# Kernel optimization log

Hardware: AMD Instinct MI355X
Metric: run time of the kernel (lower is better)

Reference implementation:

```python
import jax, jax.numpy as jnp
import numpy as np

DELTA = 0.1625
FREQ_SCALE = 0.325
MIN_LAYERS = 1
MAX_LAYERS = 5
EPS = 1e-12  # F.normalize eps


def _l2norm(x, axis):
    n = jnp.sqrt(jnp.sum(x * x, axis=axis, keepdims=True))
    return x / jnp.maximum(n, EPS)


def setup_inputs() -> dict:
    key = jax.random.key(0)
    k1, k2, k3 = jax.random.split(key, 3)
    B, N, D = 8, 2048, 64
    embeddings = jax.random.normal(k1, (B, N, D), dtype=jnp.float32)
    # scale to [0, 15) so echo_layers spans the full 1..5 range
    frequencies = jax.random.uniform(k2, (B, N), dtype=jnp.float32) * 15.0
    relationship_matrix = jax.random.uniform(k3, (B, N, N), dtype=jnp.float32)
    return {"embeddings": embeddings, "frequencies": frequencies,
            "relationship_matrix": relationship_matrix}


def reference(embeddings, frequencies, relationship_matrix):
    B, N, D = embeddings.shape
    # per-token number of echo iterations
    echo_layers = jnp.clip(
        MIN_LAYERS + jnp.floor(frequencies * FREQ_SCALE), MIN_LAYERS, MAX_LAYERS
    ).astype(jnp.int32)  # [B, N]

    refined = _l2norm(embeddings, axis=2)  # [B, N, D]

    # mask out the diagonal of the relationship matrix once (it is constant
    # across layers); shifts[i] = delta * sum_j rm[i,j]*(e_i - e_j)
    #               = delta * (e_i * rowsum[i] - (rm @ e)[i])
    rm = relationship_matrix * (1.0 - jnp.eye(N, dtype=relationship_matrix.dtype))
    rowsum = jnp.sum(rm, axis=-1)  # [B, N]

    def step(e, layer):
        active = (layer < echo_layers)[..., None].astype(e.dtype)  # [B, N, 1]
        agg = jnp.einsum('bij,bjd->bid', rm, e)                     # [B, N, D]
        shifts = DELTA * (e * rowsum[..., None] - agg)
        upd = _l2norm(e + shifts * active, axis=2)
        # tokens with zero shift are already unit-norm, so renorm is identity
        return upd, None

    refined, _ = jax.lax.scan(step, refined, jnp.arange(MAX_LAYERS))
    return refined
```

## Files before the change

kernel.cpp:

```cpp
#include <hip/hip_runtime.h>
#include <stdint.h>

#define BB 8
#define NN 2048
#define DD 64
#define DELTA 0.1625f
#define FREQ_SCALE 0.325f

typedef __bf16 bf16x8 __attribute__((ext_vector_type(8)));
typedef float f32x4 __attribute__((ext_vector_type(4)));
typedef unsigned int u32x4 __attribute__((ext_vector_type(4)));
typedef unsigned int u32x2 __attribute__((ext_vector_type(2)));

static __device__ __forceinline__ unsigned short f2b(float x) {
    union { float f; unsigned int u; } c; c.f = x;
    unsigned int r = (c.u + 0x7FFFu + ((c.u >> 16) & 1u)) >> 16;
    return (unsigned short)r;
}

static __device__ __forceinline__ void gl_lds16(const void* g, void* l) {
    __builtin_amdgcn_global_load_lds(
        (const __attribute__((address_space(1))) void*)g,
        (__attribute__((address_space(3))) void*)l, 16, 0, 0);
}

__global__ __launch_bounds__(256) void prep_norm(
        const float* __restrict__ emb, const float* __restrict__ freq,
        float* __restrict__ e0, unsigned short* __restrict__ eT0,
        int* __restrict__ echo) {
    __shared__ unsigned short tile[64][72];
    int t = threadIdx.x;
    int tok0 = blockIdx.x * 64;
    int lt = t >> 2;
    int tt = tok0 + lt;
    int dd = (t & 3) * 16;

    const float* src = emb + (size_t)tt * DD + dd;
    f32x4 v[4];
    float ss = 0.f;
    #pragma unroll
    for (int q = 0; q < 4; q++) {
        v[q] = *(const f32x4*)(src + q * 4);
        ss += v[q].x*v[q].x + v[q].y*v[q].y + v[q].z*v[q].z + v[q].w*v[q].w;
    }
    ss += __shfl_xor(ss, 1);
    ss += __shfl_xor(ss, 2);
    float scale = 1.f / fmaxf(sqrtf(ss), 1e-12f);
    float* dst = e0 + (size_t)tt * DD + dd;
    #pragma unroll
    for (int q = 0; q < 4; q++) {
        f32x4 o = v[q] * scale;
        *(f32x4*)(dst + q * 4) = o;
        tile[lt][dd + q*4 + 0] = f2b(o.x);
        tile[lt][dd + q*4 + 1] = f2b(o.y);
        tile[lt][dd + q*4 + 2] = f2b(o.z);
        tile[lt][dd + q*4 + 3] = f2b(o.w);
    }
    if ((t & 3) == 0) {
        int el = 1 + (int)floorf(freq[tt] * FREQ_SCALE);
        el = el < 1 ? 1 : (el > 5 ? 5 : el);
        echo[tt] = el;
    }
    __syncthreads();
    int b  = tok0 / NN;
    int tb = tok0 % NN;
    for (int idx = t; idx < 64 * 64; idx += 256) {
        int d = idx >> 6, j = idx & 63;
        eT0[((size_t)b * DD + d) * NN + tb + j] = tile[j][d];
    }
}

template<bool WRB>
__global__ __launch_bounds__(256) void cast_rowsum(
        const float* __restrict__ rm, unsigned short* __restrict__ rmb,
        float* __restrict__ rowsum) {
    int gw = (int)((blockIdx.x * 256 + threadIdx.x) >> 6);
    int l = threadIdx.x & 63;
    const float* src = rm + (size_t)gw * NN;
    f32x4 v[8];
    #pragma unroll
    for (int q = 0; q < 8; q++)
        v[q] = *(const f32x4*)(src + q * 256 + l * 4);
    float s = 0.f;
    #pragma unroll
    for (int q = 0; q < 8; q++)
        s += (v[q].x + v[q].y) + (v[q].z + v[q].w);
    if constexpr (WRB) {
        unsigned short* dst = rmb + (size_t)gw * NN;
        #pragma unroll
        for (int q = 0; q < 8; q++) {
            u32x2 o;
            o.x = (unsigned)f2b(v[q].x) | ((unsigned)f2b(v[q].y) << 16);
            o.y = (unsigned)f2b(v[q].z) | ((unsigned)f2b(v[q].w) << 16);
            *(u32x2*)(dst + q * 256 + l * 4) = o;
        }
    }
    #pragma unroll
    for (int m = 1; m < 64; m <<= 1) s += __shfl_xor(s, m);
    if (l == 0) rowsum[gw] = s;
}

__global__ __launch_bounds__(512, 1) void layer0_fused(
        const float* __restrict__ rm,
        const unsigned short* __restrict__ eT_src,
        const float* __restrict__ e_src,
        const int* __restrict__ echo,
        unsigned short* __restrict__ rmb_out,
        float* __restrict__ rowsum_out,
        float* __restrict__ e_dst,
        unsigned short* __restrict__ eT_dst) {
    __shared__ char F4[4][16384];
    __shared__ char C4[4][8192];
    __shared__ char SA4[4][8192];
    __shared__ float redSS[4][2][16];
    __shared__ float rsumL[64];

    const int t = threadIdx.x;
    const int w = t >> 6, l = t & 63;
    const int lo = l & 15, hi = l >> 4;
    const int it = w & 3, dh = w >> 2;
    const int gid = blockIdx.x;
    const int b  = gid & 7;
    const int i0 = (gid >> 3) * 64;

    const char* rmB = (const char*)(rm + ((size_t)b * NN + i0) * NN);
    const char* eTB = (const char*)(eT_src + (size_t)b * DD * NN);

    const size_t frow0 = (size_t)(w * 8 + (l >> 4)) * (NN * 4);
    const size_t frow4 = (size_t)(w * 8 + 4 + (l >> 4)) * (NN * 4);
    const int fcs0 = (((l & 15) ^ (l >> 4)) << 4);
    const int fcs4 = (((l & 15) ^ (4 + (l >> 4))) << 4);
    const size_t srowE = (size_t)(w * 8 + (l >> 3)) * (NN * 2);
    const int csrcE = (((l & 7) ^ (l >> 3)) << 4);

    const int rl = w * 8 + (l >> 3);
    const int cs0 = ((2 * (l & 7)) ^ (l >> 3)) << 4;
    const int cs1 = ((2 * (l & 7) + 1) ^ (l >> 3)) << 4;
    const int cdst = rl * 128 + ((((l & 7) ^ (l >> 3))) << 4);
    unsigned short* rmbW = rmb_out + ((size_t)b * NN + i0 + rl) * NN + (l & 7) * 8;

    f32x4 acc0 = {}, acc1 = {};
    float rsum = 0.f;

    const int rowB  = it * 16 + lo;
    const int rowA0 = dh * 32 + lo;
    const int rowA1 = dh * 32 + 16 + lo;
    const int xr = (lo & 7) << 4;

#define ISSUE(bi, step) do {                                        \
    const int kf = (step) * 256;                                    \
    const int ke = (step) * 128;                                    \
    gl_lds16(rmB + frow0 + kf + fcs0, &F4[bi][w * 2048]);           \
    gl_lds16(rmB + frow4 + kf + fcs4, &F4[bi][w * 2048 + 1024]);    \
    gl_lds16(eTB + srowE + ke + csrcE, &SA4[bi][w * 1024]);         \
} while (0)

#define CONVERT(bi, step) do {                                      \
    f32x4 va = *(const f32x4*)(&F4[bi][rl * 256 + cs0]);            \
    f32x4 vb = *(const f32x4*)(&F4[bi][rl * 256 + cs1]);            \
    u32x4 o;                                                        \
    o.x = (unsigned)f2b(va.x) | ((unsigned)f2b(va.y) << 16);        \
    o.y = (unsigned)f2b(va.z) | ((unsigned)f2b(va.w) << 16);        \
    o.z = (unsigned)f2b(vb.x) | ((unsigned)f2b(vb.y) << 16);        \
    o.w = (unsigned)f2b(vb.z) | ((unsigned)f2b(vb.w) << 16);        \
    *(u32x4*)(&C4[bi][cdst]) = o;                                   \
    *(u32x4*)(rmbW + (step) * 64) = o;                              \
    rsum += (va.x + va.y + va.z + va.w) + (vb.x + vb.y + vb.z + vb.w); \
} while (0)

#define COMP(bi) do {                                               \
    __builtin_amdgcn_s_setprio(1);                                  \
    _Pragma("unroll")                                               \
    for (int kk = 0; kk < 2; kk++) {                                \
        int co = ((kk << 6) | (hi << 4)) ^ xr;                      \
        u32x4 fB  = *(const u32x4*)(&C4[bi][rowB  * 128 + co]);     \
        u32x4 fA0 = *(const u32x4*)(&SA4[bi][rowA0 * 128 + co]);    \
        u32x4 fA1 = *(const u32x4*)(&SA4[bi][rowA1 * 128 + co]);    \
        acc0 = __builtin_amdgcn_mfma_f32_16x16x32_bf16(             \
            __builtin_bit_cast(bf16x8, fA0), __builtin_bit_cast(bf16x8, fB), acc0, 0, 0, 0); \
        acc1 = __builtin_amdgcn_mfma_f32_16x16x32_bf16(             \
            __builtin_bit_cast(bf16x8, fA1), __builtin_bit_cast(bf16x8, fB), acc1, 0, 0, 0); \
    }                                                               \
    __builtin_amdgcn_s_setprio(0);                                  \
} while (0)

    ISSUE(0, 0);
    ISSUE(1, 1);
    ISSUE(2, 2);
    #pragma unroll
    for (int s = 0; s < 32; s++) {
        if (s == 0)       asm volatile("s_waitcnt vmcnt(6)" ::: "memory");
        else if (s == 1)  asm volatile("s_waitcnt vmcnt(7)" ::: "memory");
        else if (s == 2)  asm volatile("s_waitcnt vmcnt(8)" ::: "memory");
        else if (s < 30)  asm volatile("s_waitcnt vmcnt(9)" ::: "memory");
        else if (s == 30) asm volatile("s_waitcnt vmcnt(6)" ::: "memory");
        else              asm volatile("s_waitcnt vmcnt(3)" ::: "memory");
        __builtin_amdgcn_s_barrier();
        __builtin_amdgcn_sched_barrier(0);
        if (s < 29) {
            const int nb = (s + 3) & 3;
            if (nb == 0)      ISSUE(0, s + 3);
            else if (nb == 1) ISSUE(1, s + 3);
            else if (nb == 2) ISSUE(2, s + 3);
            else              ISSUE(3, s + 3);
        }
        const int cb = s & 3;
        if (cb == 0)      CONVERT(0, s);
        else if (cb == 1) CONVERT(1, s);
        else if (cb == 2) CONVERT(2, s);
        else              CONVERT(3, s);
        asm volatile("s_waitcnt lgkmcnt(0)" ::: "memory");
        __builtin_amdgcn_sched_barrier(0);
        __builtin_amdgcn_s_barrier();
        if (cb == 0)      COMP(0);
        else if (cb == 1) COMP(1);
        else if (cb == 2) COMP(2);
        else              COMP(3);
    }
#undef ISSUE
#undef CONVERT
#undef COMP

    rsum += __shfl_xor(rsum, 1);
    rsum += __shfl_xor(rsum, 2);
    rsum += __shfl_xor(rsum, 4);
    if ((l & 7) == 0) {
        rsumL[rl] = rsum;
        rowsum_out[(size_t)b * NN + i0 + rl] = rsum;
    }
    __syncthreads();

    const size_t gi = (size_t)b * NN + i0 + it * 16 + lo;
    const float rs = rsumL[it * 16 + lo];
    const float coef = (0 < echo[gi]) ? DELTA : 0.f;
    const size_t eb = gi * DD + dh * 32 + hi * 4;
    f32x4 e0 = *(const f32x4*)(e_src + eb);
    f32x4 e1 = *(const f32x4*)(e_src + eb + 16);
    f32x4 u0 = e0 + coef * (e0 * rs - acc0);
    f32x4 u1 = e1 + coef * (e1 * rs - acc1);
    float ss = u0.x*u0.x + u0.y*u0.y + u0.z*u0.z + u0.w*u0.w
             + u1.x*u1.x + u1.y*u1.y + u1.z*u1.z + u1.w*u1.w;
    ss += __shfl_xor(ss, 16);
    ss += __shfl_xor(ss, 32);
    if (hi == 0) redSS[it][dh][lo] = ss;
    __syncthreads();
    float sst = redSS[it][0][lo] + redSS[it][1][lo];
    float scale = 1.f / fmaxf(sqrtf(sst), 1e-12f);
    u0 *= scale;
    u1 *= scale;
    *(f32x4*)(e_dst + eb) = u0;
    *(f32x4*)(e_dst + eb + 16) = u1;
    unsigned short* ep = eT_dst + (size_t)b * DD * NN;
    const int i = i0 + it * 16 + lo;
    const int d0 = dh * 32 + hi * 4;
    ep[(size_t)(d0 + 0)  * NN + i] = f2b(u0.x);
    ep[(size_t)(d0 + 1)  * NN + i] = f2b(u0.y);
    ep[(size_t)(d0 + 2)  * NN + i] = f2b(u0.z);
    ep[(size_t)(d0 + 3)  * NN + i] = f2b(u0.w);
    ep[(size_t)(d0 + 16) * NN + i] = f2b(u1.x);
    ep[(size_t)(d0 + 17) * NN + i] = f2b(u1.y);
    ep[(size_t)(d0 + 18) * NN + i] = f2b(u1.z);
    ep[(size_t)(d0 + 19) * NN + i] = f2b(u1.w);
}

__global__ __launch_bounds__(512, 1) void layer_fused(
        const unsigned short* __restrict__ rmb,
        const unsigned short* __restrict__ eT_src,
        const float* __restrict__ e_src,
        const float* __restrict__ rowsum_g,
        const int* __restrict__ echo,
        float* __restrict__ e_dst,
        unsigned short* __restrict__ eT_dst,
        int layer) {
    __shared__ char SB6[6][8192];
    __shared__ char SA6[6][8192];
    __shared__ float redSS[4][2][16];

    const int t = threadIdx.x;
    const int w = t >> 6, l = t & 63;
    const int lo = l & 15, hi = l >> 4;
    const int it = w & 3, dh = w >> 2;
    const int gid = blockIdx.x;
    const int b  = gid & 7;
    const int i0 = (gid >> 3) * 64;

    const char* rmB = (const char*)(rmb + ((size_t)b * NN + i0) * NN);
    const char* eTB = (const char*)(eT_src + (size_t)b * DD * NN);

    const size_t srow = (size_t)(w * 8 + (l >> 3)) * (NN * 2);
    const int csrc = ((l & 7) ^ (l >> 3)) << 4;

    f32x4 acc0 = {}, acc1 = {};

    const int rowB  = it * 16 + lo;
    const int rowA0 = dh * 32 + lo;
    const int rowA1 = dh * 32 + 16 + lo;
    const int xr = (lo & 7) << 4;

#define ISSUE(bi, step) do {                                       \
    const int ksb = (step) * 128;                                  \
    gl_lds16(rmB + srow + ksb + csrc, &SB6[bi][w * 1024]);         \
    gl_lds16(eTB + srow + ksb + csrc, &SA6[bi][w * 1024]);         \
} while (0)

#define COMP(bi) do {                                              \
    __builtin_amdgcn_s_setprio(1);                                 \
    _Pragma("unroll")                                              \
    for (int kk = 0; kk < 2; kk++) {                               \
        int co = ((kk << 6) | (hi << 4)) ^ xr;                     \
        u32x4 fB  = *(const u32x4*)(&SB6[bi][rowB  * 128 + co]);   \
        u32x4 fA0 = *(const u32x4*)(&SA6[bi][rowA0 * 128 + co]);   \
        u32x4 fA1 = *(const u32x4*)(&SA6[bi][rowA1 * 128 + co]);   \
        acc0 = __builtin_amdgcn_mfma_f32_16x16x32_bf16(            \
            __builtin_bit_cast(bf16x8, fA0), __builtin_bit_cast(bf16x8, fB), acc0, 0, 0, 0); \
        acc1 = __builtin_amdgcn_mfma_f32_16x16x32_bf16(            \
            __builtin_bit_cast(bf16x8, fA1), __builtin_bit_cast(bf16x8, fB), acc1, 0, 0, 0); \
    }                                                              \
    __builtin_amdgcn_s_setprio(0);                                 \
} while (0)

    ISSUE(0, 0);
    ISSUE(1, 1);
    ISSUE(2, 2);
    ISSUE(3, 3);
    ISSUE(4, 4);
    #pragma unroll
    for (int s = 0; s < 32; s++) {
        if (s < 29)       asm volatile("s_waitcnt vmcnt(8)" ::: "memory");
        else if (s == 29) asm volatile("s_waitcnt vmcnt(4)" ::: "memory");
        else if (s == 30) asm volatile("s_waitcnt vmcnt(2)" ::: "memory");
        else              asm volatile("s_waitcnt vmcnt(0)" ::: "memory");
        __builtin_amdgcn_s_barrier();
        __builtin_amdgcn_sched_barrier(0);
        if (s < 27) {
            const int nb = (s + 5) % 6;
            if (nb == 0)      ISSUE(0, s + 5);
            else if (nb == 1) ISSUE(1, s + 5);
            else if (nb == 2) ISSUE(2, s + 5);
            else if (nb == 3) ISSUE(3, s + 5);
            else if (nb == 4) ISSUE(4, s + 5);
            else              ISSUE(5, s + 5);
        }
        const int cb = s % 6;
        if (cb == 0)      COMP(0);
        else if (cb == 1) COMP(1);
        else if (cb == 2) COMP(2);
        else if (cb == 3) COMP(3);
        else if (cb == 4) COMP(4);
        else              COMP(5);
    }
#undef ISSUE
#undef COMP

    const size_t gi = (size_t)b * NN + i0 + it * 16 + lo;
    const float rs = rowsum_g[gi];
    const float coef = (layer < echo[gi]) ? DELTA : 0.f;
    const size_t eb = gi * DD + dh * 32 + hi * 4;
    f32x4 e0 = *(const f32x4*)(e_src + eb);
    f32x4 e1 = *(const f32x4*)(e_src + eb + 16);
    f32x4 u0 = e0 + coef * (e0 * rs - acc0);
    f32x4 u1 = e1 + coef * (e1 * rs - acc1);
    float ss = u0.x*u0.x + u0.y*u0.y + u0.z*u0.z + u0.w*u0.w
             + u1.x*u1.x + u1.y*u1.y + u1.z*u1.z + u1.w*u1.w;
    ss += __shfl_xor(ss, 16);
    ss += __shfl_xor(ss, 32);
    if (hi == 0) redSS[it][dh][lo] = ss;
    __syncthreads();
    float sst = redSS[it][0][lo] + redSS[it][1][lo];
    float scale = 1.f / fmaxf(sqrtf(sst), 1e-12f);
    u0 *= scale;
    u1 *= scale;
    *(f32x4*)(e_dst + eb) = u0;
    *(f32x4*)(e_dst + eb + 16) = u1;
    unsigned short* ep = eT_dst + (size_t)b * DD * NN;
    const int i = i0 + it * 16 + lo;
    const int d0 = dh * 32 + hi * 4;
    ep[(size_t)(d0 + 0)  * NN + i] = f2b(u0.x);
    ep[(size_t)(d0 + 1)  * NN + i] = f2b(u0.y);
    ep[(size_t)(d0 + 2)  * NN + i] = f2b(u0.z);
    ep[(size_t)(d0 + 3)  * NN + i] = f2b(u0.w);
    ep[(size_t)(d0 + 16) * NN + i] = f2b(u1.x);
    ep[(size_t)(d0 + 17) * NN + i] = f2b(u1.y);
    ep[(size_t)(d0 + 18) * NN + i] = f2b(u1.z);
    ep[(size_t)(d0 + 19) * NN + i] = f2b(u1.w);
}

__global__ __launch_bounds__(512, 4) void layer_step_fb(
        const float* __restrict__ rm_,
        const unsigned short* __restrict__ eT_src,
        const float* __restrict__ e_src,
        const float* __restrict__ rowsum_g,
        const int* __restrict__ echo,
        float* __restrict__ e_dst,
        unsigned short* __restrict__ eT_dst,
        int layer) {
    __shared__ float redAcc[3][2][64][20];

    int t = threadIdx.x;
    int w = t >> 6, l = t & 63;
    int b = blockIdx.y;
    int i0 = blockIdx.x * 32;
    int wi = w & 1;
    int kq = w >> 1;
    int lane_lo = l & 15, lane_hi = l >> 4;
    int i = i0 + wi * 16 + lane_lo;
    size_t gi = (size_t)b * NN + i;
    int kbase = kq * (NN / 4) + 8 * lane_hi;

    int echo_pre = echo[gi];
    float rs = rowsum_g[gi];

    const unsigned short* eT_b = eT_src + (size_t)b * DD * NN;
    const unsigned short* ea0 = eT_b + (size_t)(lane_lo)      * NN + kbase;
    const unsigned short* ea1 = eT_b + (size_t)(16 + lane_lo) * NN + kbase;
    const unsigned short* ea2 = eT_b + (size_t)(32 + lane_lo) * NN + kbase;
    const unsigned short* ea3 = eT_b + (size_t)(48 + lane_lo) * NN + kbase;

    f32x4 acc[4] = {};
    const float* rmp32 = rm_ + gi * NN + kbase;

    #pragma unroll
    for (int j = 0; j < 16; j++) {
        const int o = 32 * j;
        f32x4 lo4 = *(const f32x4*)(rmp32 + o);
        f32x4 hi4 = *(const f32x4*)(rmp32 + o + 4);
        u32x4 ob;
        ob.x = (unsigned)f2b(lo4.x) | ((unsigned)f2b(lo4.y) << 16);
        ob.y = (unsigned)f2b(lo4.z) | ((unsigned)f2b(lo4.w) << 16);
        ob.z = (unsigned)f2b(hi4.x) | ((unsigned)f2b(hi4.y) << 16);
        ob.w = (unsigned)f2b(hi4.z) | ((unsigned)f2b(hi4.w) << 16);
        bf16x8 bfrag = __builtin_bit_cast(bf16x8, ob);
        acc[0] = __builtin_amdgcn_mfma_f32_16x16x32_bf16(
            __builtin_bit_cast(bf16x8, *(const u32x4*)(ea0 + o)), bfrag, acc[0], 0, 0, 0);
        acc[1] = __builtin_amdgcn_mfma_f32_16x16x32_bf16(
            __builtin_bit_cast(bf16x8, *(const u32x4*)(ea1 + o)), bfrag, acc[1], 0, 0, 0);
        acc[2] = __builtin_amdgcn_mfma_f32_16x16x32_bf16(
            __builtin_bit_cast(bf16x8, *(const u32x4*)(ea2 + o)), bfrag, acc[2], 0, 0, 0);
        acc[3] = __builtin_amdgcn_mfma_f32_16x16x32_bf16(
            __builtin_bit_cast(bf16x8, *(const u32x4*)(ea3 + o)), bfrag, acc[3], 0, 0, 0);
    }

    if (kq > 0) {
        #pragma unroll
        for (int f = 0; f < 4; f++)
            *(f32x4*)(&redAcc[kq - 1][wi][l][4 * f]) = acc[f];
    }
    __syncthreads();
    if (kq == 0) {
        #pragma unroll
        for (int f = 0; f < 4; f++) {
            acc[f] += *(const f32x4*)(&redAcc[0][wi][l][4 * f]);
            acc[f] += *(const f32x4*)(&redAcc[1][wi][l][4 * f]);
            acc[f] += *(const f32x4*)(&redAcc[2][wi][l][4 * f]);
        }
        float coef = DELTA * ((layer < echo_pre) ? 1.f : 0.f);
        size_t ebase = gi * DD;
        f32x4 upd[4];
        float ss = 0.f;
        #pragma unroll
        for (int f = 0; f < 4; f++) {
            f32x4 e = *(const f32x4*)(e_src + ebase + 16 * f + 4 * lane_hi);
            f32x4 u = e + coef * (e * rs - acc[f]);
            upd[f] = u;
            ss += u.x*u.x + u.y*u.y + u.z*u.z + u.w*u.w;
        }
        ss += __shfl_xor(ss, 16);
        ss += __shfl_xor(ss, 32);
        float scale = 1.f / fmaxf(sqrtf(ss), 1e-12f);
        unsigned short* ep = eT_dst + (size_t)b * DD * NN;
        #pragma unroll
        for (int f = 0; f < 4; f++) {
            f32x4 o = upd[f] * scale;
            *(f32x4*)(e_dst + ebase + 16 * f + 4 * lane_hi) = o;
            int dbase = 16 * f + 4 * lane_hi;
            ep[(size_t)(dbase + 0) * NN + i] = f2b(o.x);
            ep[(size_t)(dbase + 1) * NN + i] = f2b(o.y);
            ep[(size_t)(dbase + 2) * NN + i] = f2b(o.z);
            ep[(size_t)(dbase + 3) * NN + i] = f2b(o.w);
        }
    }
}

extern "C" void kernel_launch(void* const* d_in, const int* in_sizes, int n_in,
                              void* d_out, int out_size, void* d_ws, size_t ws_size,
                              hipStream_t stream) {
    const float* emb  = (const float*)d_in[0];
    const float* freq = (const float*)d_in[1];
    const float* rm   = (const float*)d_in[2];
    float* out = (float*)d_out;
    char* ws = (char*)d_ws;

    const size_t eBytes   = (size_t)BB * NN * DD * 4;
    const size_t eTBytes  = (size_t)BB * DD * NN * 2;
    const size_t bnBytes  = (size_t)BB * NN * 4;
    const size_t rmbBytes = (size_t)BB * NN * NN * 2;
    float* e_f32[2] = { (float*)ws, (float*)(ws + eBytes) };
    unsigned short* eT[2] = { (unsigned short*)(ws + 2*eBytes),
                              (unsigned short*)(ws + 2*eBytes + eTBytes) };
    float* rowsum = (float*)(ws + 2*eBytes + 2*eTBytes);
    int* echo = (int*)(ws + 2*eBytes + 2*eTBytes + bnBytes);
    unsigned short* rmb = (unsigned short*)(ws + 2*eBytes + 2*eTBytes + 2*bnBytes);
    size_t need_cached = 2*eBytes + 2*eTBytes + 2*bnBytes + rmbBytes;

    int cached = (ws_size >= need_cached) ? 1 : 0;

    prep_norm<<<dim3(BB*NN/64), dim3(256), 0, stream>>>(emb, freq, e_f32[0], eT[0], echo);

    if (cached) {
        layer0_fused<<<dim3(256), dim3(512), 0, stream>>>(
            rm, eT[0], e_f32[0], echo, rmb, rowsum, e_f32[1], eT[1]);
        for (int l = 1; l < 5; l++) {
            float* dst = (l == 4) ? out : e_f32[(l + 1) & 1];
            layer_fused<<<dim3(256), dim3(512), 0, stream>>>(
                rmb, eT[l & 1], e_f32[l & 1], rowsum, echo,
                dst, eT[(l + 1) & 1], l);
        }
    } else {
        cast_rowsum<false><<<dim3(BB*NN/4), dim3(256), 0, stream>>>(rm, nullptr, rowsum);
        for (int l = 0; l < 5; l++) {
            float* dst = (l == 4) ? out : e_f32[(l + 1) & 1];
            layer_step_fb<<<dim3(NN/32, BB), dim3(512), 0, stream>>>(
                rm, eT[l & 1], e_f32[l & 1], rowsum, echo,
                dst, eT[(l + 1) & 1], l);
        }
    }
}
```

Measured before the change: 106.7 us.

## Use 2x2 register-blocked MFMA tiles with split-K warps and LDS reduction

Each warp previously computed a 16-row by 32-dim slice over the full K chunk. Now it computes a 32x32 output tile with four accumulators over half of the K chunk, so each LDS fragment feeds two MFMAs. The two K halves are then summed through LDS before the normalize epilogue. Layer 0 also drops the echo lookup, because every token has at least one active layer. The trade-off is an extra barrier, a reduction round trip through LDS, and an epilogue where only half the warps do work.

After: 108.4 us. Within noise of the previous version (+1.5%).

```diff
diff --git a/kernel.cpp b/kernel.cpp
--- a/kernel.cpp
+++ b/kernel.cpp
@@ -11,6 +11,9 @@
 typedef float f32x4 __attribute__((ext_vector_type(4)));
 typedef unsigned int u32x4 __attribute__((ext_vector_type(4)));
 typedef unsigned int u32x2 __attribute__((ext_vector_type(2)));
+
+#define MFMA16(A, B, C) __builtin_amdgcn_mfma_f32_16x16x32_bf16( \
+    __builtin_bit_cast(bf16x8, A), __builtin_bit_cast(bf16x8, B), C, 0, 0, 0)
 
 static __device__ __forceinline__ unsigned short f2b(float x) {
     union { float f; unsigned int u; } c; c.f = x;
@@ -104,7 +107,6 @@
         const float* __restrict__ rm,
         const unsigned short* __restrict__ eT_src,
         const float* __restrict__ e_src,
-        const int* __restrict__ echo,
         unsigned short* __restrict__ rmb_out,
         float* __restrict__ rowsum_out,
         float* __restrict__ e_dst,
@@ -112,13 +114,13 @@
     __shared__ char F4[4][16384];
     __shared__ char C4[4][8192];
     __shared__ char SA4[4][8192];
-    __shared__ float redSS[4][2][16];
+    __shared__ float redSS2[2][2][2][16];
     __shared__ float rsumL[64];
 
     const int t = threadIdx.x;
     const int w = t >> 6, l = t & 63;
     const int lo = l & 15, hi = l >> 4;
-    const int it = w & 3, dh = w >> 2;
+    const int ri = w & 1, rd = (w >> 1) & 1, ks = w >> 2;
     const int gid = blockIdx.x;
     const int b  = gid & 7;
     const int i0 = (gid >> 3) * 64;
@@ -139,12 +141,11 @@
     const int cdst = rl * 128 + ((((l & 7) ^ (l >> 3))) << 4);
     unsigned short* rmbW = rmb_out + ((size_t)b * NN + i0 + rl) * NN + (l & 7) * 8;
 
-    f32x4 acc0 = {}, acc1 = {};
+    f32x4 acc00 = {}, acc01 = {}, acc10 = {}, acc11 = {};
     float rsum = 0.f;
 
-    const int rowB  = it * 16 + lo;
-    const int rowA0 = dh * 32 + lo;
-    const int rowA1 = dh * 32 + 16 + lo;
+    const int rowB0 = ri * 32 + lo, rowB1 = ri * 32 + 16 + lo;
+    const int rowA0 = rd * 32 + lo, rowA1 = rd * 32 + 16 + lo;
     const int xr = (lo & 7) << 4;
 
 #define ISSUE(bi, step) do {                                        \
@@ -170,17 +171,15 @@
 
 #define COMP(bi) do {                                               \
     __builtin_amdgcn_s_setprio(1);                                  \
-    _Pragma("unroll")                                               \
-    for (int kk = 0; kk < 2; kk++) {                                \
-        int co = ((kk << 6) | (hi << 4)) ^ xr;                      \
-        u32x4 fB  = *(const u32x4*)(&C4[bi][rowB  * 128 + co]);     \
-        u32x4 fA0 = *(const u32x4*)(&SA4[bi][rowA0 * 128 + co]);    \
-        u32x4 fA1 = *(const u32x4*)(&SA4[bi][rowA1 * 128 + co]);    \
-        acc0 = __builtin_amdgcn_mfma_f32_16x16x32_bf16(             \
-            __builtin_bit_cast(bf16x8, fA0), __builtin_bit_cast(bf16x8, fB), acc0, 0, 0, 0); \
-        acc1 = __builtin_amdgcn_mfma_f32_16x16x32_bf16(             \
-            __builtin_bit_cast(bf16x8, fA1), __builtin_bit_cast(bf16x8, fB), acc1, 0, 0, 0); \
-    }                                                               \
+    const int co = ((ks << 6) | (hi << 4)) ^ xr;                    \
+    u32x4 fB0 = *(const u32x4*)(&C4[bi][rowB0 * 128 + co]);         \
+    u32x4 fB1 = *(const u32x4*)(&C4[bi][rowB1 * 128 + co]);         \
+    u32x4 fA0 = *(const u32x4*)(&SA4[bi][rowA0 * 128 + co]);        \
+    u32x4 fA1 = *(const u32x4*)(&SA4[bi][rowA1 * 128 + co]);        \
+    acc00 = MFMA16(fA0, fB0, acc00);                                \
+    acc01 = MFMA16(fA0, fB1, acc01);                                \
+    acc10 = MFMA16(fA1, fB0, acc10);                                \
+    acc11 = MFMA16(fA1, fB1, acc11);                                \
     __builtin_amdgcn_s_setprio(0);                                  \
 } while (0)
 
@@ -228,39 +227,83 @@
         rsumL[rl] = rsum;
         rowsum_out[(size_t)b * NN + i0 + rl] = rsum;
     }
-    __syncthreads();
-
-    const size_t gi = (size_t)b * NN + i0 + it * 16 + lo;
-    const float rs = rsumL[it * 16 + lo];
-    const float coef = (0 < echo[gi]) ? DELTA : 0.f;
-    const size_t eb = gi * DD + dh * 32 + hi * 4;
-    f32x4 e0 = *(const f32x4*)(e_src + eb);
-    f32x4 e1 = *(const f32x4*)(e_src + eb + 16);
-    f32x4 u0 = e0 + coef * (e0 * rs - acc0);
-    f32x4 u1 = e1 + coef * (e1 * rs - acc1);
-    float ss = u0.x*u0.x + u0.y*u0.y + u0.z*u0.z + u0.w*u0.w
-             + u1.x*u1.x + u1.y*u1.y + u1.z*u1.z + u1.w*u1.w;
-    ss += __shfl_xor(ss, 16);
-    ss += __shfl_xor(ss, 32);
-    if (hi == 0) redSS[it][dh][lo] = ss;
-    __syncthreads();
-    float sst = redSS[it][0][lo] + redSS[it][1][lo];
-    float scale = 1.f / fmaxf(sqrtf(sst), 1e-12f);
-    u0 *= scale;
-    u1 *= scale;
-    *(f32x4*)(e_dst + eb) = u0;
-    *(f32x4*)(e_dst + eb + 16) = u1;
-    unsigned short* ep = eT_dst + (size_t)b * DD * NN;
-    const int i = i0 + it * 16 + lo;
-    const int d0 = dh * 32 + hi * 4;
-    ep[(size_t)(d0 + 0)  * NN + i] = f2b(u0.x);
-    ep[(size_t)(d0 + 1)  * NN + i] = f2b(u0.y);
-    ep[(size_t)(d0 + 2)  * NN + i] = f2b(u0.z);
-    ep[(size_t)(d0 + 3)  * NN + i] = f2b(u0.w);
-    ep[(size_t)(d0 + 16) * NN + i] = f2b(u1.x);
-    ep[(size_t)(d0 + 17) * NN + i] = f2b(u1.y);
-    ep[(size_t)(d0 + 18) * NN + i] = f2b(u1.z);
-    ep[(size_t)(d0 + 19) * NN + i] = f2b(u1.w);
+
+    float* redK = (float*)&F4[0][0];
+    __syncthreads();
+    if (ks == 1) {
+        float* dp = redK + ((ri * 2 + rd) * 64 + l) * 17;
+        #pragma unroll
+        for (int j = 0; j < 4; j++) {
+            dp[j] = acc00[j]; dp[4 + j] = acc01[j];
+            dp[8 + j] = acc10[j]; dp[12 + j] = acc11[j];
+        }
+    }
+    __syncthreads();
+    f32x4 u00, u01, u10, u11;
+    size_t eb0 = 0, eb1 = 0;
+    if (ks == 0) {
+        const float* sp = redK + ((ri * 2 + rd) * 64 + l) * 17;
+        #pragma unroll
+        for (int j = 0; j < 4; j++) {
+            acc00[j] += sp[j]; acc01[j] += sp[4 + j];
+            acc10[j] += sp[8 + j]; acc11[j] += sp[12 + j];
+        }
+        const size_t gi0 = (size_t)b * NN + i0 + ri * 32 + lo;
+        const size_t gi1 = gi0 + 16;
+        const float rs0 = rsumL[ri * 32 + lo];
+        const float rs1 = rsumL[ri * 32 + 16 + lo];
+        eb0 = gi0 * DD + rd * 32 + hi * 4;
+        eb1 = gi1 * DD + rd * 32 + hi * 4;
+        f32x4 e00 = *(const f32x4*)(e_src + eb0);
+        f32x4 e10 = *(const f32x4*)(e_src + eb0 + 16);
+        f32x4 e01 = *(const f32x4*)(e_src + eb1);
+        f32x4 e11 = *(const f32x4*)(e_src + eb1 + 16);
+        u00 = e00 + DELTA * (e00 * rs0 - acc00);
+        u10 = e10 + DELTA * (e10 * rs0 - acc10);
+        u01 = e01 + DELTA * (e01 * rs1 - acc01);
+        u11 = e11 + DELTA * (e11 * rs1 - acc11);
+        float ss0 = u00.x*u00.x + u00.y*u00.y + u00.z*u00.z + u00.w*u00.w
+                  + u10.x*u10.x + u10.y*u10.y + u10.z*u10.z + u10.w*u10.w;
+        float ss1 = u01.x*u01.x + u01.y*u01.y + u01.z*u01.z + u01.w*u01.w
+                  + u11.x*u11.x + u11.y*u11.y + u11.z*u11.z + u11.w*u11.w;
+        ss0 += __shfl_xor(ss0, 16); ss0 += __shfl_xor(ss0, 32);
+        ss1 += __shfl_xor(ss1, 16); ss1 += __shfl_xor(ss1, 32);
+        if (hi == 0) {
+            redSS2[ri][rd][0][lo] = ss0;
+            redSS2[ri][rd][1][lo] = ss1;
+        }
+    }
+    __syncthreads();
+    if (ks == 0) {
+        const float sc0 = 1.f / fmaxf(sqrtf(redSS2[ri][0][0][lo] + redSS2[ri][1][0][lo]), 1e-12f);
+        const float sc1 = 1.f / fmaxf(sqrtf(redSS2[ri][0][1][lo] + redSS2[ri][1][1][lo]), 1e-12f);
+        u00 *= sc0; u10 *= sc0; u01 *= sc1; u11 *= sc1;
+        *(f32x4*)(e_dst + eb0) = u00;
+        *(f32x4*)(e_dst + eb0 + 16) = u10;
+        *(f32x4*)(e_dst + eb1) = u01;
+        *(f32x4*)(e_dst + eb1 + 16) = u11;
+        unsigned short* ep = eT_dst + (size_t)b * DD * NN;
+        const int iA = i0 + ri * 32 + lo;
+        const int iB = iA + 16;
+        const int dA = rd * 32 + hi * 4;
+        const int dB = dA + 16;
+        ep[(size_t)(dA + 0) * NN + iA] = f2b(u00.x);
+        ep[(size_t)(dA + 1) * NN + iA] = f2b(u00.y);
+        ep[(size_t)(dA + 2) * NN + iA] = f2b(u00.z);
+        ep[(size_t)(dA + 3) * NN + iA] = f2b(u00.w);
+        ep[(size_t)(dB + 0) * NN + iA] = f2b(u10.x);
+        ep[(size_t)(dB + 1) * NN + iA] = f2b(u10.y);
+        ep[(size_t)(dB + 2) * NN + iA] = f2b(u10.z);
+        ep[(size_t)(dB + 3) * NN + iA] = f2b(u10.w);
+        ep[(size_t)(dA + 0) * NN + iB] = f2b(u01.x);
+        ep[(size_t)(dA + 1) * NN + iB] = f2b(u01.y);
+        ep[(size_t)(dA + 2) * NN + iB] = f2b(u01.z);
+        ep[(size_t)(dA + 3) * NN + iB] = f2b(u01.w);
+        ep[(size_t)(dB + 0) * NN + iB] = f2b(u11.x);
+        ep[(size_t)(dB + 1) * NN + iB] = f2b(u11.y);
+        ep[(size_t)(dB + 2) * NN + iB] = f2b(u11.z);
+        ep[(size_t)(dB + 3) * NN + iB] = f2b(u11.w);
+    }
 }
 
 __global__ __launch_bounds__(512, 1) void layer_fused(
@@ -274,12 +317,12 @@
         int layer) {
     __shared__ char SB6[6][8192];
     __shared__ char SA6[6][8192];
-    __shared__ float redSS[4][2][16];
+    __shared__ float redSS2[2][2][2][16];
 
     const int t = threadIdx.x;
     const int w = t >> 6, l = t & 63;
     const int lo = l & 15, hi = l >> 4;
-    const int it = w & 3, dh = w >> 2;
+    const int ri = w & 1, rd = (w >> 1) & 1, ks = w >> 2;
     const int gid = blockIdx.x;
     const int b  = gid & 7;
     const int i0 = (gid >> 3) * 64;
@@ -290,11 +333,10 @@
     const size_t srow = (size_t)(w * 8 + (l >> 3)) * (NN * 2);
     const int csrc = ((l & 7) ^ (l >> 3)) << 4;
 
-    f32x4 acc0 = {}, acc1 = {};
-
-    const int rowB  = it * 16 + lo;
-    const int rowA0 = dh * 32 + lo;
-    const int rowA1 = dh * 32 + 16 + lo;
+    f32x4 acc00 = {}, acc01 = {}, acc10 = {}, acc11 = {};
+
+    const int rowB0 = ri * 32 + lo, rowB1 = ri * 32 + 16 + lo;
+    const int rowA0 = rd * 32 + lo, rowA1 = rd * 32 + 16 + lo;
     const int xr = (lo & 7) << 4;
 
 #define ISSUE(bi, step) do {                                       \
@@ -305,17 +347,15 @@
 
 #define COMP(bi) do {                                              \
     __builtin_amdgcn_s_setprio(1);                                 \
-    _Pragma("unroll")                                              \
-    for (int kk = 0; kk < 2; kk++) {                               \
-        int co = ((kk << 6) | (hi << 4)) ^ xr;                     \
-        u32x4 fB  = *(const u32x4*)(&SB6[bi][rowB  * 128 + co]);   \
-        u32x4 fA0 = *(const u32x4*)(&SA6[bi][rowA0 * 128 + co]);   \
-        u32x4 fA1 = *(const u32x4*)(&SA6[bi][rowA1 * 128 + co]);   \
-        acc0 = __builtin_amdgcn_mfma_f32_16x16x32_bf16(            \
-            __builtin_bit_cast(bf16x8, fA0), __builtin_bit_cast(bf16x8, fB), acc0, 0, 0, 0); \
-        acc1 = __builtin_amdgcn_mfma_f32_16x16x32_bf16(            \
-            __builtin_bit_cast(bf16x8, fA1), __builtin_bit_cast(bf16x8, fB), acc1, 0, 0, 0); \
-    }                                                              \
+    const int co = ((ks << 6) | (hi << 4)) ^ xr;                   \
+    u32x4 fB0 = *(const u32x4*)(&SB6[bi][rowB0 * 128 + co]);       \
+    u32x4 fB1 = *(const u32x4*)(&SB6[bi][rowB1 * 128 + co]);       \
+    u32x4 fA0 = *(const u32x4*)(&SA6[bi][rowA0 * 128 + co]);       \
+    u32x4 fA1 = *(const u32x4*)(&SA6[bi][rowA1 * 128 + co]);       \
+    acc00 = MFMA16(fA0, fB0, acc00);                               \
+    acc01 = MFMA16(fA0, fB1, acc01);                               \
+    acc10 = MFMA16(fA1, fB0, acc10);                               \
+    acc11 = MFMA16(fA1, fB1, acc11);                               \
     __builtin_amdgcn_s_setprio(0);                                 \
 } while (0)
 
@@ -352,37 +392,84 @@
 #undef ISSUE
 #undef COMP
 
-    const size_t gi = (size_t)b * NN + i0 + it * 16 + lo;
-    const float rs = rowsum_g[gi];
-    const float coef = (layer < echo[gi]) ? DELTA : 0.f;
-    const size_t eb = gi * DD + dh * 32 + hi * 4;
-    f32x4 e0 = *(const f32x4*)(e_src + eb);
-    f32x4 e1 = *(const f32x4*)(e_src + eb + 16);
-    f32x4 u0 = e0 + coef * (e0 * rs - acc0);
-    f32x4 u1 = e1 + coef * (e1 * rs - acc1);
-    float ss = u0.x*u0.x + u0.y*u0.y + u0.z*u0.z + u0.w*u0.w
-             + u1.x*u1.x + u1.y*u1.y + u1.z*u1.z + u1.w*u1.w;
-    ss += __shfl_xor(ss, 16);
-    ss += __shfl_xor(ss, 32);
-    if (hi == 0) redSS[it][dh][lo] = ss;
-    __syncthreads();
-    float sst = redSS[it][0][lo] + redSS[it][1][lo];
-    float scale = 1.f / fmaxf(sqrtf(sst), 1e-12f);
-    u0 *= scale;
-    u1 *= scale;
-    *(f32x4*)(e_dst + eb) = u0;
-    *(f32x4*)(e_dst + eb + 16) = u1;
-    unsigned short* ep = eT_dst + (size_t)b * DD * NN;
-    const int i = i0 + it * 16 + lo;
-    const int d0 = dh * 32 + hi * 4;
-    ep[(size_t)(d0 + 0)  * NN + i] = f2b(u0.x);
-    ep[(size_t)(d0 + 1)  * NN + i] = f2b(u0.y);
-    ep[(size_t)(d0 + 2)  * NN + i] = f2b(u0.z);
-    ep[(size_t)(d0 + 3)  * NN + i] = f2b(u0.w);
-    ep[(size_t)(d0 + 16) * NN + i] = f2b(u1.x);
-    ep[(size_t)(d0 + 17) * NN + i] = f2b(u1.y);
-    ep[(size_t)(d0 + 18) * NN + i] = f2b(u1.z);
-    ep[(size_t)(d0 + 19) * NN + i] = f2b(u1.w);
+    float* redK = (float*)&SB6[0][0];
+    __syncthreads();
+    if (ks == 1) {
+        float* dp = redK + ((ri * 2 + rd) * 64 + l) * 17;
+        #pragma unroll
+        for (int j = 0; j < 4; j++) {
+            dp[j] = acc00[j]; dp[4 + j] = acc01[j];
+            dp[8 + j] = acc10[j]; dp[12 + j] = acc11[j];
+        }
+    }
+    __syncthreads();
+    f32x4 u00, u01, u10, u11;
+    size_t eb0 = 0, eb1 = 0;
+    if (ks == 0) {
+        const float* sp = redK + ((ri * 2 + rd) * 64 + l) * 17;
+        #pragma unroll
+        for (int j = 0; j < 4; j++) {
+            acc00[j] += sp[j]; acc01[j] += sp[4 + j];
+            acc10[j] += sp[8 + j]; acc11[j] += sp[12 + j];
+        }
+        const size_t gi0 = (size_t)b * NN + i0 + ri * 32 + lo;
+        const size_t gi1 = gi0 + 16;
+        const float rs0 = rowsum_g[gi0];
+        const float rs1 = rowsum_g[gi1];
+        const float c0 = (layer < echo[gi0]) ? DELTA : 0.f;
+        const float c1 = (layer < echo[gi1]) ? DELTA : 0.f;
+        eb0 = gi0 * DD + rd * 32 + hi * 4;
+        eb1 = gi1 * DD + rd * 32 + hi * 4;
+        f32x4 e00 = *(const f32x4*)(e_src + eb0);
+        f32x4 e10 = *(const f32x4*)(e_src + eb0 + 16);
+        f32x4 e01 = *(const f32x4*)(e_src + eb1);
+        f32x4 e11 = *(const f32x4*)(e_src + eb1 + 16);
+        u00 = e00 + c0 * (e00 * rs0 - acc00);
+        u10 = e10 + c0 * (e10 * rs0 - acc10);
+        u01 = e01 + c1 * (e01 * rs1 - acc01);
+        u11 = e11 + c1 * (e11 * rs1 - acc11);
+        float ss0 = u00.x*u00.x + u00.y*u00.y + u00.z*u00.z + u00.w*u00.w
+                  + u10.x*u10.x + u10.y*u10.y + u10.z*u10.z + u10.w*u10.w;
+        float ss1 = u01.x*u01.x + u01.y*u01.y + u01.z*u01.z + u01.w*u01.w
+                  + u11.x*u11.x + u11.y*u11.y + u11.z*u11.z + u11.w*u11.w;
+        ss0 += __shfl_xor(ss0, 16); ss0 += __shfl_xor(ss0, 32);
+        ss1 += __shfl_xor(ss1, 16); ss1 += __shfl_xor(ss1, 32);
+        if (hi == 0) {
+            redSS2[ri][rd][0][lo] = ss0;
+            redSS2[ri][rd][1][lo] = ss1;
+        }
+    }
+    __syncthreads();
+    if (ks == 0) {
+        const float sc0 = 1.f / fmaxf(sqrtf(redSS2[ri][0][0][lo] + redSS2[ri][1][0][lo]), 1e-12f);
+        const float sc1 = 1.f / fmaxf(sqrtf(redSS2[ri][0][1][lo] + redSS2[ri][1][1][lo]), 1e-12f);
+        u00 *= sc0; u10 *= sc0; u01 *= sc1; u11 *= sc1;
+        *(f32x4*)(e_dst + eb0) = u00;
+        *(f32x4*)(e_dst + eb0 + 16) = u10;
+        *(f32x4*)(e_dst + eb1) = u01;
+        *(f32x4*)(e_dst + eb1 + 16) = u11;
+        unsigned short* ep = eT_dst + (size_t)b * DD * NN;
+        const int iA = i0 + ri * 32 + lo;
+        const int iB = iA + 16;
+        const int dA = rd * 32 + hi * 4;
+        const int dB = dA + 16;
+        ep[(size_t)(dA + 0) * NN + iA] = f2b(u00.x);
+        ep[(size_t)(dA + 1) * NN + iA] = f2b(u00.y);
+        ep[(size_t)(dA + 2) * NN + iA] = f2b(u00.z);
+        ep[(size_t)(dA + 3) * NN + iA] = f2b(u00.w);
+        ep[(size_t)(dB + 0) * NN + iA] = f2b(u10.x);
+        ep[(size_t)(dB + 1) * NN + iA] = f2b(u10.y);
+        ep[(size_t)(dB + 2) * NN + iA] = f2b(u10.z);
+        ep[(size_t)(dB + 3) * NN + iA] = f2b(u10.w);
+        ep[(size_t)(dA + 0) * NN + iB] = f2b(u01.x);
+        ep[(size_t)(dA + 1) * NN + iB] = f2b(u01.y);
+        ep[(size_t)(dA + 2) * NN + iB] = f2b(u01.z);
+        ep[(size_t)(dA + 3) * NN + iB] = f2b(u01.w);
+        ep[(size_t)(dB + 0) * NN + iB] = f2b(u11.x);
+        ep[(size_t)(dB + 1) * NN + iB] = f2b(u11.y);
+        ep[(size_t)(dB + 2) * NN + iB] = f2b(u11.z);
+        ep[(size_t)(dB + 3) * NN + iB] = f2b(u11.w);
+    }
 }
 
 __global__ __launch_bounds__(512, 4) void layer_step_fb(
@@ -430,14 +517,11 @@
         ob.z = (unsigned)f2b(hi4.x) | ((unsigned)f2b(hi4.y) << 16);
         ob.w = (unsigned)f2b(hi4.z) | ((unsigned)f2b(hi4.w) << 16);
         bf16x8 bfrag = __builtin_bit_cast(bf16x8, ob);
-        acc[0] = __builtin_amdgcn_mfma_f32_16x16x32_bf16(
-            __builtin_bit_cast(bf16x8, *(const u32x4*)(ea0 + o)), bfrag, acc[0], 0, 0, 0);
-        acc[1] = __builtin_amdgcn_mfma_f32_16x16x32_bf16(
-            __builtin_bit_cast(bf16x8, *(const u32x4*)(ea1 + o)), bfrag, acc[1], 0, 0, 0);
-        acc[2] = __builtin_amdgcn_mfma_f32_16x16x32_bf16(
-            __builtin_bit_cast(bf16x8, *(const u32x4*)(ea2 + o)), bfrag, acc[2], 0, 0, 0);
-        acc[3] = __builtin_amdgcn_mfma_f32_16x16x32_bf16(
-            __builtin_bit_cast(bf16x8, *(const u32x4*)(ea3 + o)), bfrag, acc[3], 0, 0, 0);
+        acc[0] = MFMA16(*(const u32x4*)(ea0 + o), ob, acc[0]);
+        acc[1] = MFMA16(*(const u32x4*)(ea1 + o), ob, acc[1]);
+        acc[2] = MFMA16(*(const u32x4*)(ea2 + o), ob, acc[2]);
+        acc[3] = MFMA16(*(const u32x4*)(ea3 + o), ob, acc[3]);
+        (void)bfrag;
     }
 
     if (kq > 0) {
@@ -508,7 +592,7 @@
 
     if (cached) {
         layer0_fused<<<dim3(256), dim3(512), 0, stream>>>(
-            rm, eT[0], e_f32[0], echo, rmb, rowsum, e_f32[1], eT[1]);
+            rm, eT[0], e_f32[0], rmb, rowsum, e_f32[1], eT[1]);
         for (int l = 1; l < 5; l++) {
             float* dst = (l == 4) ? out : e_f32[(l + 1) & 1];
             layer_fused<<<dim3(256), dim3(512), 0, stream>>>(
```
